# Kernel tuning notes

Measured on AMD Instinct MI355X. Metric: run time of the kernel, lower is better.

## Reference

```python
import jax, jax.numpy as jnp
import numpy as np

D_MODEL, D_K, D_V = 1024, 128, 128
B, S = 8, 2048


def setup_inputs() -> dict:
    key = jax.random.key(0)
    ks = jax.random.split(key, 10)
    scale = 1.0 / np.sqrt(D_MODEL)
    return {
        "inputs_q": jax.random.normal(ks[0], (B, S, D_MODEL), jnp.float32),
        "inputs_k": jax.random.normal(ks[1], (B, S, D_MODEL), jnp.float32),
        "inputs_v": jax.random.normal(ks[2], (B, S, D_MODEL), jnp.float32),
        "mask": jax.random.randint(ks[3], (B, 1, S), 0, 2, jnp.int32),
        "Wq": jax.random.normal(ks[4], (D_MODEL, D_K), jnp.float32) * scale,
        "bq": jnp.zeros((D_K,), jnp.float32),
        "Wk": jax.random.normal(ks[5], (D_MODEL, D_K), jnp.float32) * scale,
        "bk": jnp.zeros((D_K,), jnp.float32),
        "Wv": jax.random.normal(ks[6], (D_MODEL, D_V), jnp.float32) * scale,
        "bv": jnp.zeros((D_V,), jnp.float32),
    }


def reference(inputs_q, inputs_k, inputs_v, mask, Wq, bq, Wk, bk, Wv, bv):
    query = inputs_q @ Wq + bq            # [B,Sq,d_k]
    key = inputs_k @ Wk + bk              # [B,Sk,d_k]
    value = inputs_v @ Wv + bv            # [B,Sk,d_v]
    scores = jnp.einsum('bqd,bkd->bqk', query, key) / jnp.sqrt(jnp.float32(D_K))
    # original: mask==True means attend; inverted mask positions get -1e9
    mask_float = jnp.logical_not(mask.astype(bool)).astype(jnp.float32)  # [B,1,Sk]
    scores = scores + mask_float * (-1e9)
    attention_weights = jax.nn.softmax(scores, axis=-1)
    attention_weights = attention_weights * (1.0 - mask_float)
    output = jnp.einsum('bqk,bkv->bqv', attention_weights, value)
    return output
```

## Files before the change

kernel.cpp:

```cpp
#include <hip/hip_runtime.h>

#define L2E 1.44269504088896341f
#define SM_SHIFT 5.77078016355585f

typedef _Float16 h8 __attribute__((ext_vector_type(8)));
typedef float f4 __attribute__((ext_vector_type(4)));

__device__ __forceinline__ void gll16(const void* g, void* l) {
  __builtin_amdgcn_global_load_lds((const __attribute__((address_space(1))) void*)g,
                                   (__attribute__((address_space(3))) void*)l, 16, 0, 0);
}

__device__ __forceinline__ f4 mfma_h(h8 a, h8 b, f4 c) {
  return __builtin_amdgcn_mfma_f32_16x16x32_f16(a, b, c, 0, 0, 0);
}

__device__ __forceinline__ h8 pack8(const float4& a, const float4& b) {
  h8 hv;
  hv[0] = (_Float16)a.x; hv[1] = (_Float16)a.y; hv[2] = (_Float16)a.z; hv[3] = (_Float16)a.w;
  hv[4] = (_Float16)b.x; hv[5] = (_Float16)b.y; hv[6] = (_Float16)b.z; hv[7] = (_Float16)b.w;
  return hv;
}

__global__ void wt_prep(const float* __restrict__ Wq, const float* __restrict__ Wk,
                        const float* __restrict__ Wv, const int* __restrict__ maskp,
                        _Float16* __restrict__ Wt, _Float16* __restrict__ mh) {
  int z = blockIdx.y;
  const float* W = (z == 0) ? Wq : ((z == 1) ? Wk : Wv);
  _Float16* o = Wt + (size_t)z * 131072;
  int idx = blockIdx.x * 256 + threadIdx.x;
  int k = idx >> 7, n = idx & 127;
  o[(k >> 6) * 8192 + ((k >> 3) & 7) * 1024 + n * 8 + (k & 7)] = (_Float16)W[idx];
  if (z == 0 && idx < 16384) mh[idx] = (_Float16)(float)maskp[idx];
}

__global__ __launch_bounds__(256) void proj_qkv(
    const float* __restrict__ Xq, const float* __restrict__ Xk, const float* __restrict__ Xv,
    const _Float16* __restrict__ Wt, const int* __restrict__ maskp,
    const float* __restrict__ bq, const float* __restrict__ bk, const float* __restrict__ bv,
    _Float16* __restrict__ Qh, _Float16* __restrict__ Kpk, _Float16* __restrict__ Vpk) {
  const int z = blockIdx.y;
  const float* X; const float* bias;
  if (z == 0) { X = Xq; bias = bq; }
  else if (z == 1) { X = Xk; bias = bk; }
  else { X = Xv; bias = bv; }
  const _Float16* Wz = Wt + (size_t)z * 131072;
  const int row0 = blockIdx.x * 64;
  const int tid = threadIdx.x;
  const int lane = tid & 63, wid = tid >> 6;
  const int wr = wid >> 1, wc = wid & 1;
  const int l15 = lane & 15, g = lane >> 4;

  __shared__ __align__(16) _Float16 Al[2][4096];
  __shared__ __align__(16) _Float16 Bl[2][8192];

  f4 acc[2][4];
#pragma unroll
  for (int i = 0; i < 2; i++)
#pragma unroll
    for (int j = 0; j < 4; j++) acc[i][j] = (f4){0.f, 0.f, 0.f, 0.f};

  float4 areg[2][2];

#pragma unroll
  for (int it = 0; it < 2; it++) {
    int c = it * 256 + tid; int r = c >> 3, kb = c & 7;
    const float* gp = X + (row0 + r) * 1024 + kb * 8;
    areg[it][0] = *(const float4*)gp;
    areg[it][1] = *(const float4*)(gp + 4);
  }
#pragma unroll
  for (int it = 0; it < 4; it++)
    gll16(Wz + it * 2048 + tid * 8, &Bl[0][it * 2048 + tid * 8]);
#pragma unroll
  for (int it = 0; it < 2; it++) {
    int c = it * 256 + tid; int r = c >> 3, kb = c & 7;
    *(h8*)&Al[0][(kb * 64 + r) * 8] = pack8(areg[it][0], areg[it][1]);
  }
  __syncthreads();

  int cur = 0;
  for (int kt = 0; kt < 16; kt++) {
    if (kt < 15) {
#pragma unroll
      for (int it = 0; it < 2; it++) {
        int c = it * 256 + tid; int r = c >> 3, kb = c & 7;
        const float* gp = X + (row0 + r) * 1024 + (kt + 1) * 64 + kb * 8;
        areg[it][0] = *(const float4*)gp;
        areg[it][1] = *(const float4*)(gp + 4);
      }
#pragma unroll
      for (int it = 0; it < 4; it++)
        gll16(Wz + (kt + 1) * 8192 + it * 2048 + tid * 8, &Bl[cur ^ 1][it * 2048 + tid * 8]);
    }
#pragma unroll
    for (int k0 = 0; k0 < 2; k0++) {
      h8 af[2], bf[4];
      int kb = k0 * 4 + g;
#pragma unroll
      for (int mf = 0; mf < 2; mf++) {
        int row = wr * 32 + mf * 16 + l15;
        af[mf] = *(const h8*)&Al[cur][(kb * 64 + row) * 8];
      }
#pragma unroll
      for (int nf = 0; nf < 4; nf++) {
        int col = wc * 64 + nf * 16 + l15;
        bf[nf] = *(const h8*)&Bl[cur][(kb * 128 + col) * 8];
      }
#pragma unroll
      for (int mf = 0; mf < 2; mf++)
#pragma unroll
        for (int nf = 0; nf < 4; nf++)
          acc[mf][nf] = mfma_h(af[mf], bf[nf], acc[mf][nf]);
    }
    if (kt < 15) {
      asm volatile("s_waitcnt vmcnt(0)" ::: "memory");
#pragma unroll
      for (int it = 0; it < 2; it++) {
        int c = it * 256 + tid; int r = c >> 3, kb = c & 7;
        *(h8*)&Al[cur ^ 1][(kb * 64 + r) * 8] = pack8(areg[it][0], areg[it][1]);
      }
    }
    __syncthreads();
    cur ^= 1;
  }

  const float qscale = (z == 0) ? 0.08838834764831845f : 1.0f;
#pragma unroll
  for (int mf = 0; mf < 2; mf++)
#pragma unroll
    for (int nf = 0; nf < 4; nf++) {
      int colb = wc * 64 + nf * 16 + l15;
      float bv_ = bias[colb];
#pragma unroll
      for (int jj = 0; jj < 4; jj++) {
        int row = wr * 32 + mf * 16 + g * 4 + jj;
        int m = row0 + row;
        float v = (acc[mf][nf][jj] + bv_) * qscale;
        if (z == 2) v *= (float)maskp[m];
        _Float16 hv = (_Float16)v;
        if (z == 0) Qh[m * 128 + colb] = hv;
        else if (z == 1) Kpk[(m >> 6) * 8192 + (colb >> 3) * 512 + (m & 63) * 8 + (colb & 7)] = hv;
        else Vpk[(m >> 6) * 8192 + ((m & 63) >> 3) * 1024 + colb * 8 + (m & 7)] = hv;
      }
    }
}

__global__ __launch_bounds__(256) void attn_fwd(
    const _Float16* __restrict__ Qh, const _Float16* __restrict__ Kpk,
    const _Float16* __restrict__ Vpk, const _Float16* __restrict__ maskh,
    float* __restrict__ Out) {
  const int bi = blockIdx.x & 7;
  const int qt = blockIdx.x >> 3;
  const int tid = threadIdx.x;
  const int lane = tid & 63, wid = tid >> 6;
  const int l15 = lane & 15, g = lane >> 4;

  __shared__ __align__(16) _Float16 Kt[2][16384];
  __shared__ __align__(16) _Float16 Vt[2][16384];
  __shared__ __align__(16) _Float16 Pl[4][2048];
  __shared__ __align__(16) _Float16 Ml[2][128];

  const size_t mb = (size_t)bi * 2048;
  const int q0 = qt * 64 + wid * 16;

  h8 qf[4];
#pragma unroll
  for (int c = 0; c < 4; c++)
    qf[c] = *(const h8*)(Qh + (mb + q0 + l15) * 128 + c * 32 + g * 8);

  const _Float16* Kb = Kpk + (size_t)bi * 262144;
  const _Float16* Vb = Vpk + (size_t)bi * 262144;
  const _Float16* mhp = maskh + mb;

  f4 oacc[8];
#pragma unroll
  for (int i = 0; i < 8; i++) oacc[i] = (f4){0.f, 0.f, 0.f, 0.f};
  f4 lacc = (f4){0.f, 0.f, 0.f, 0.f};

  auto stage = [&](int buf, int s) {
    const _Float16* gk = Kb + (size_t)s * 16384;
    const _Float16* gv = Vb + (size_t)s * 16384;
#pragma unroll
    for (int it = 0; it < 8; it++) {
      gll16(gk + (it * 256 + tid) * 8, &Kt[buf][(it * 256 + tid) * 8]);
      gll16(gv + (it * 256 + tid) * 8, &Vt[buf][(it * 256 + tid) * 8]);
    }
    if (lane < 16) gll16(mhp + s * 128 + lane * 8, &Ml[buf][lane * 8]);
  };

  stage(0, 0);

  int cur = 0;
  for (int s = 0; s < 16; s++) {
    asm volatile("s_waitcnt vmcnt(0)" ::: "memory");
    __syncthreads();
    if (s < 15) stage(cur ^ 1, s + 1);

    f4 sc[8];
#pragma unroll
    for (int nf = 0; nf < 8; nf++) sc[nf] = (f4){0.f, 0.f, 0.f, 0.f};
#pragma unroll
    for (int c = 0; c < 4; c++) {
      int dblk = c * 4 + g;
#pragma unroll
      for (int nf = 0; nf < 8; nf++) {
        int key = nf * 16 + l15;
        h8 bfr = *(const h8*)&Kt[cur][(key >> 6) * 8192 + ((dblk * 64 + (key & 63)) << 3)];
        sc[nf] = mfma_h(qf[c], bfr, sc[nf]);
      }
    }

#pragma unroll
    for (int nf = 0; nf < 8; nf++) {
      int key = nf * 16 + l15;
      int kb = key >> 3, j = key & 7;
#pragma unroll
      for (int jj = 0; jj < 4; jj++) {
        int q = g * 4 + jj;
        float p = __builtin_amdgcn_exp2f(sc[nf][jj] * L2E - SM_SHIFT);
        Pl[wid][((kb * 16 + (q ^ (kb & 7))) << 3) + j] = (_Float16)p;
      }
    }

#pragma unroll
    for (int kc = 0; kc < 4; kc++) {
      int kb = kc * 4 + g;
      h8 pa = *(const h8*)&Pl[wid][((kb * 16 + (l15 ^ (kb & 7))) << 3)];
      h8 mfr = *(const h8*)&Ml[cur][kc * 32 + g * 8];
      lacc = mfma_h(pa, mfr, lacc);
#pragma unroll
      for (int nf = 0; nf < 8; nf++) {
        int d = nf * 16 + l15;
        h8 va = *(const h8*)&Vt[cur][(kc >> 1) * 8192 + ((((kc & 1) * 4 + g) * 128 + d) << 3)];
        oacc[nf] = mfma_h(pa, va, oacc[nf]);
      }
    }
    cur ^= 1;
  }

  float inv[4];
#pragma unroll
  for (int jj = 0; jj < 4; jj++)
    inv[jj] = (lacc[jj] > 0.f) ? 1.0f / lacc[jj] : 0.0f;
#pragma unroll
  for (int nf = 0; nf < 8; nf++)
#pragma unroll
    for (int jj = 0; jj < 4; jj++)
      Out[(mb + q0 + g * 4 + jj) * 128 + nf * 16 + l15] = oacc[nf][jj] * inv[jj];
}

extern "C" void kernel_launch(void* const* d_in, const int* in_sizes, int n_in,
                              void* d_out, int out_size, void* d_ws, size_t ws_size,
                              hipStream_t stream) {
  const float* Xq = (const float*)d_in[0];
  const float* Xk = (const float*)d_in[1];
  const float* Xv = (const float*)d_in[2];
  const int* mask = (const int*)d_in[3];
  const float* Wq = (const float*)d_in[4];
  const float* bq = (const float*)d_in[5];
  const float* Wk = (const float*)d_in[6];
  const float* bk = (const float*)d_in[7];
  const float* Wv = (const float*)d_in[8];
  const float* bv = (const float*)d_in[9];
  float* Out = (float*)d_out;

  char* ws = (char*)d_ws;
  _Float16* Qh    = (_Float16*)(ws);
  _Float16* Kpk   = (_Float16*)(ws + 4194304);
  _Float16* Vpk   = (_Float16*)(ws + 8388608);
  _Float16* Wt    = (_Float16*)(ws + 12582912);
  _Float16* maskh = (_Float16*)(ws + 13369344);

  wt_prep<<<dim3(512, 3), 256, 0, stream>>>(Wq, Wk, Wv, mask, Wt, maskh);
  proj_qkv<<<dim3(256, 3), 256, 0, stream>>>(Xq, Xk, Xv, Wt, mask, bq, bk, bv, Qh, Kpk, Vpk);
  attn_fwd<<<dim3(256), 256, 0, stream>>>(Qh, Kpk, Vpk, maskh, Out);
}
```

Baseline: 94.29 us.

## Replace LDS-direct async loads with register-staged prefetch and XOR-swizzled LDS

```diff
diff --git a/kernel.cpp b/kernel.cpp
--- a/kernel.cpp
+++ b/kernel.cpp
@@ -5,11 +5,6 @@
 
 typedef _Float16 h8 __attribute__((ext_vector_type(8)));
 typedef float f4 __attribute__((ext_vector_type(4)));
-
-__device__ __forceinline__ void gll16(const void* g, void* l) {
-  __builtin_amdgcn_global_load_lds((const __attribute__((address_space(1))) void*)g,
-                                   (__attribute__((address_space(3))) void*)l, 16, 0, 0);
-}
 
 __device__ __forceinline__ f4 mfma_h(h8 a, h8 b, f4 c) {
   return __builtin_amdgcn_mfma_f32_16x16x32_f16(a, b, c, 0, 0, 0);
@@ -34,7 +29,7 @@
   if (z == 0 && idx < 16384) mh[idx] = (_Float16)(float)maskp[idx];
 }
 
-__global__ __launch_bounds__(256) void proj_qkv(
+__global__ __launch_bounds__(128) void proj_qkv(
     const float* __restrict__ Xq, const float* __restrict__ Xk, const float* __restrict__ Xv,
     const _Float16* __restrict__ Wt, const int* __restrict__ maskp,
     const float* __restrict__ bq, const float* __restrict__ bk, const float* __restrict__ bv,
@@ -48,94 +43,72 @@
   const int row0 = blockIdx.x * 64;
   const int tid = threadIdx.x;
   const int lane = tid & 63, wid = tid >> 6;
-  const int wr = wid >> 1, wc = wid & 1;
   const int l15 = lane & 15, g = lane >> 4;
 
-  __shared__ __align__(16) _Float16 Al[2][4096];
-  __shared__ __align__(16) _Float16 Bl[2][8192];
-
-  f4 acc[2][4];
+  __shared__ __align__(16) _Float16 Bl[8192];
+
+  const float* a0 = X + (size_t)(row0 + wid * 32 + l15) * 1024 + g * 8;
+  const float* a1 = a0 + 16 * 1024;
+
+  f4 acc[2][8];
 #pragma unroll
   for (int i = 0; i < 2; i++)
 #pragma unroll
-    for (int j = 0; j < 4; j++) acc[i][j] = (f4){0.f, 0.f, 0.f, 0.f};
-
-  float4 areg[2][2];
-
-#pragma unroll
-  for (int it = 0; it < 2; it++) {
-    int c = it * 256 + tid; int r = c >> 3, kb = c & 7;
-    const float* gp = X + (row0 + r) * 1024 + kb * 8;
-    areg[it][0] = *(const float4*)gp;
-    areg[it][1] = *(const float4*)(gp + 4);
-  }
-#pragma unroll
-  for (int it = 0; it < 4; it++)
-    gll16(Wz + it * 2048 + tid * 8, &Bl[0][it * 2048 + tid * 8]);
-#pragma unroll
-  for (int it = 0; it < 2; it++) {
-    int c = it * 256 + tid; int r = c >> 3, kb = c & 7;
-    *(h8*)&Al[0][(kb * 64 + r) * 8] = pack8(areg[it][0], areg[it][1]);
-  }
-  __syncthreads();
-
-  int cur = 0;
-  for (int kt = 0; kt < 16; kt++) {
-    if (kt < 15) {
-#pragma unroll
-      for (int it = 0; it < 2; it++) {
-        int c = it * 256 + tid; int r = c >> 3, kb = c & 7;
-        const float* gp = X + (row0 + r) * 1024 + (kt + 1) * 64 + kb * 8;
-        areg[it][0] = *(const float4*)gp;
-        areg[it][1] = *(const float4*)(gp + 4);
-      }
-#pragma unroll
-      for (int it = 0; it < 4; it++)
-        gll16(Wz + (kt + 1) * 8192 + it * 2048 + tid * 8, &Bl[cur ^ 1][it * 2048 + tid * 8]);
-    }
-#pragma unroll
-    for (int k0 = 0; k0 < 2; k0++) {
-      h8 af[2], bf[4];
-      int kb = k0 * 4 + g;
-#pragma unroll
-      for (int mf = 0; mf < 2; mf++) {
-        int row = wr * 32 + mf * 16 + l15;
-        af[mf] = *(const h8*)&Al[cur][(kb * 64 + row) * 8];
-      }
-#pragma unroll
-      for (int nf = 0; nf < 4; nf++) {
-        int col = wc * 64 + nf * 16 + l15;
-        bf[nf] = *(const h8*)&Bl[cur][(kb * 128 + col) * 8];
-      }
-#pragma unroll
-      for (int mf = 0; mf < 2; mf++)
-#pragma unroll
-        for (int nf = 0; nf < 4; nf++)
-          acc[mf][nf] = mfma_h(af[mf], bf[nf], acc[mf][nf]);
-    }
-    if (kt < 15) {
-      asm volatile("s_waitcnt vmcnt(0)" ::: "memory");
-#pragma unroll
-      for (int it = 0; it < 2; it++) {
-        int c = it * 256 + tid; int r = c >> 3, kb = c & 7;
-        *(h8*)&Al[cur ^ 1][(kb * 64 + r) * 8] = pack8(areg[it][0], areg[it][1]);
-      }
-    }
-    __syncthreads();
-    cur ^= 1;
+    for (int j = 0; j < 8; j++) acc[i][j] = (f4){0.f, 0.f, 0.f, 0.f};
+
+  h8 breg[8];
+#pragma unroll
+  for (int it = 0; it < 8; it++)
+    breg[it] = *(const h8*)(Wz + (it * 128 + tid) * 8);
+
+  for (int t = 0; t < 16; t++) {
+#pragma unroll
+    for (int it = 0; it < 8; it++)
+      *(h8*)&Bl[(it * 128 + (tid ^ (it & 7))) * 8] = breg[it];
+    __syncthreads();
+
+    float4 ar[8];
+    {
+      const float* pa = a0 + t * 64;
+      ar[0] = *(const float4*)pa;        ar[1] = *(const float4*)(pa + 4);
+      ar[2] = *(const float4*)(pa + 32); ar[3] = *(const float4*)(pa + 36);
+      const float* pb = a1 + t * 64;
+      ar[4] = *(const float4*)pb;        ar[5] = *(const float4*)(pb + 4);
+      ar[6] = *(const float4*)(pb + 32); ar[7] = *(const float4*)(pb + 36);
+    }
+    if (t < 15) {
+#pragma unroll
+      for (int it = 0; it < 8; it++)
+        breg[it] = *(const h8*)(Wz + (t + 1) * 8192 + (it * 128 + tid) * 8);
+    }
+#pragma unroll
+    for (int kc = 0; kc < 2; kc++) {
+      int kb = kc * 4 + g;
+      h8 bf[8];
+#pragma unroll
+      for (int nf = 0; nf < 8; nf++)
+        bf[nf] = *(const h8*)&Bl[(kb * 128 + ((nf * 16 + l15) ^ (kb & 7))) * 8];
+      h8 af0 = pack8(ar[kc * 2], ar[kc * 2 + 1]);
+      h8 af1 = pack8(ar[4 + kc * 2], ar[5 + kc * 2]);
+#pragma unroll
+      for (int nf = 0; nf < 8; nf++) {
+        acc[0][nf] = mfma_h(af0, bf[nf], acc[0][nf]);
+        acc[1][nf] = mfma_h(af1, bf[nf], acc[1][nf]);
+      }
+    }
+    __syncthreads();
   }
 
   const float qscale = (z == 0) ? 0.08838834764831845f : 1.0f;
 #pragma unroll
-  for (int mf = 0; mf < 2; mf++)
-#pragma unroll
-    for (int nf = 0; nf < 4; nf++) {
-      int colb = wc * 64 + nf * 16 + l15;
-      float bv_ = bias[colb];
+  for (int nf = 0; nf < 8; nf++) {
+    int colb = nf * 16 + l15;
+    float bv_ = bias[colb];
+#pragma unroll
+    for (int mf = 0; mf < 2; mf++)
 #pragma unroll
       for (int jj = 0; jj < 4; jj++) {
-        int row = wr * 32 + mf * 16 + g * 4 + jj;
-        int m = row0 + row;
+        int m = row0 + wid * 32 + mf * 16 + g * 4 + jj;
         float v = (acc[mf][nf][jj] + bv_) * qscale;
         if (z == 2) v *= (float)maskp[m];
         _Float16 hv = (_Float16)v;
@@ -143,7 +116,7 @@
         else if (z == 1) Kpk[(m >> 6) * 8192 + (colb >> 3) * 512 + (m & 63) * 8 + (colb & 7)] = hv;
         else Vpk[(m >> 6) * 8192 + ((m & 63) >> 3) * 1024 + colb * 8 + (m & 7)] = hv;
       }
-    }
+  }
 }
 
 __global__ __launch_bounds__(256) void attn_fwd(
@@ -156,10 +129,9 @@
   const int lane = tid & 63, wid = tid >> 6;
   const int l15 = lane & 15, g = lane >> 4;
 
-  __shared__ __align__(16) _Float16 Kt[2][16384];
-  __shared__ __align__(16) _Float16 Vt[2][16384];
+  __shared__ __align__(16) _Float16 Kt[16384];
+  __shared__ __align__(16) _Float16 Vt[16384];
   __shared__ __align__(16) _Float16 Pl[4][2048];
-  __shared__ __align__(16) _Float16 Ml[2][128];
 
   const size_t mb = (size_t)bi * 2048;
   const int q0 = qt * 64 + wid * 16;
@@ -178,24 +150,31 @@
   for (int i = 0; i < 8; i++) oacc[i] = (f4){0.f, 0.f, 0.f, 0.f};
   f4 lacc = (f4){0.f, 0.f, 0.f, 0.f};
 
-  auto stage = [&](int buf, int s) {
-    const _Float16* gk = Kb + (size_t)s * 16384;
-    const _Float16* gv = Vb + (size_t)s * 16384;
+  h8 kreg[8], vreg[8];
+#pragma unroll
+  for (int it = 0; it < 8; it++) {
+    kreg[it] = *(const h8*)(Kb + (it * 256 + tid) * 8);
+    vreg[it] = *(const h8*)(Vb + (it * 256 + tid) * 8);
+  }
+
+  for (int s = 0; s < 16; s++) {
 #pragma unroll
     for (int it = 0; it < 8; it++) {
-      gll16(gk + (it * 256 + tid) * 8, &Kt[buf][(it * 256 + tid) * 8]);
-      gll16(gv + (it * 256 + tid) * 8, &Vt[buf][(it * 256 + tid) * 8]);
-    }
-    if (lane < 16) gll16(mhp + s * 128 + lane * 8, &Ml[buf][lane * 8]);
-  };
-
-  stage(0, 0);
-
-  int cur = 0;
-  for (int s = 0; s < 16; s++) {
-    asm volatile("s_waitcnt vmcnt(0)" ::: "memory");
-    __syncthreads();
-    if (s < 15) stage(cur ^ 1, s + 1);
+      int wg = it * 256 + tid;
+      *(h8*)&Kt[(wg ^ ((wg >> 6) & 7)) * 8] = kreg[it];
+      *(h8*)&Vt[(wg ^ ((wg >> 7) & 7)) * 8] = vreg[it];
+    }
+    __syncthreads();
+
+    if (s < 15) {
+      const _Float16* gk = Kb + (size_t)(s + 1) * 16384;
+      const _Float16* gv = Vb + (size_t)(s + 1) * 16384;
+#pragma unroll
+      for (int it = 0; it < 8; it++) {
+        kreg[it] = *(const h8*)(gk + (it * 256 + tid) * 8);
+        vreg[it] = *(const h8*)(gv + (it * 256 + tid) * 8);
+      }
+    }
 
     f4 sc[8];
 #pragma unroll
@@ -206,7 +185,8 @@
 #pragma unroll
       for (int nf = 0; nf < 8; nf++) {
         int key = nf * 16 + l15;
-        h8 bfr = *(const h8*)&Kt[cur][(key >> 6) * 8192 + ((dblk * 64 + (key & 63)) << 3)];
+        int kg = (key >> 6) * 1024 + dblk * 64 + ((key & 63) ^ (dblk & 7));
+        h8 bfr = *(const h8*)&Kt[kg * 8];
         sc[nf] = mfma_h(qf[c], bfr, sc[nf]);
       }
     }
@@ -227,16 +207,18 @@
     for (int kc = 0; kc < 4; kc++) {
       int kb = kc * 4 + g;
       h8 pa = *(const h8*)&Pl[wid][((kb * 16 + (l15 ^ (kb & 7))) << 3)];
-      h8 mfr = *(const h8*)&Ml[cur][kc * 32 + g * 8];
+      h8 mfr = *(const h8*)(mhp + s * 128 + kc * 32 + g * 8);
       lacc = mfma_h(pa, mfr, lacc);
+      int rbl = (kc & 1) * 4 + g;
 #pragma unroll
       for (int nf = 0; nf < 8; nf++) {
         int d = nf * 16 + l15;
-        h8 va = *(const h8*)&Vt[cur][(kc >> 1) * 8192 + ((((kc & 1) * 4 + g) * 128 + d) << 3)];
+        int vg = (kc >> 1) * 1024 + rbl * 128 + (d ^ (rbl & 7));
+        h8 va = *(const h8*)&Vt[vg * 8];
         oacc[nf] = mfma_h(pa, va, oacc[nf]);
       }
     }
-    cur ^= 1;
+    __syncthreads();
   }
 
   float inv[4];
@@ -273,6 +255,6 @@
   _Float16* maskh = (_Float16*)(ws + 13369344);
 
   wt_prep<<<dim3(512, 3), 256, 0, stream>>>(Wq, Wk, Wv, mask, Wt, maskh);
-  proj_qkv<<<dim3(256, 3), 256, 0, stream>>>(Xq, Xk, Xv, Wt, mask, bq, bk, bv, Qh, Kpk, Vpk);
+  proj_qkv<<<dim3(256, 3), 128, 0, stream>>>(Xq, Xk, Xv, Wt, mask, bq, bk, bv, Qh, Kpk, Vpk);
   attn_fwd<<<dim3(256), 256, 0, stream>>>(Qh, Kpk, Vpk, maskh, Out);
 }
```

Result: slower. 121.1 us (+28.4%).
